# Optimization experiments

Hardware: AMD Instinct MI355X
Metric: run time of the kernel (lower is better)

Reference implementation:

```python
import jax, jax.numpy as jnp
import numpy as np
from functools import partial

B = 524288      # batch
CH = 30         # channel_num (input dim)
FEA = 42        # feature dim consumed by all classifiers
HID = 64        # assumed hidden width of the (unshown) Feature MLP
NC = 2          # num_class -> number of conditional-domain experts
ND = 6          # num_domain
ALPHA = 1.0

# Gradient Reversal Layer: identity fwd, -alpha * grad bwd
@partial(jax.custom_vjp, nondiff_argnums=(1,))
def grl(x, alpha):
    return x

def _grl_fwd(x, alpha):
    return x, None

def _grl_bwd(alpha, res, g):
    return (-alpha * g,)

grl.defvjp(_grl_fwd, _grl_bwd)


def setup_inputs() -> dict:
    key = jax.random.key(0)
    ks = jax.random.split(key, 24)
    r = lambda k, shape, s=0.1: (jax.random.normal(k, shape, dtype=jnp.float32) * s)
    inp = {
        "x": jax.random.normal(ks[0], (B, CH), dtype=jnp.float32),
        "y": jax.random.randint(ks[1], (B,), 0, NC, dtype=jnp.int32),
        # Feature MLP (assumed: CH -> HID -> FEA with ReLU)
        "W_f1": r(ks[2], (CH, HID)), "b_f1": jnp.zeros((HID,), jnp.float32),
        "W_f2": r(ks[3], (HID, FEA)), "b_f2": jnp.zeros((FEA,), jnp.float32),
        # TaskClassifier: 42 -> 20 -> NC
        "W_t1": r(ks[4], (FEA, 20)), "b_t1": jnp.zeros((20,), jnp.float32),
        "W_t2": r(ks[5], (20, NC)), "b_t2": jnp.zeros((NC,), jnp.float32),
        # prior domain classifier: 42 -> 20 -> 20 -> ND
        "W_p1": r(ks[6], (FEA, 20)), "b_p1": jnp.zeros((20,), jnp.float32),
        "W_p2": r(ks[7], (20, 20)), "b_p2": jnp.zeros((20,), jnp.float32),
        "W_p3": r(ks[8], (20, ND)), "b_p3": jnp.zeros((ND,), jnp.float32),
        # NC conditional domain experts, stacked: [NC, ...]
        "W_c1": r(ks[9], (NC, FEA, 20)), "b_c1": jnp.zeros((NC, 20), jnp.float32),
        "W_c2": r(ks[10], (NC, 20, 20)), "b_c2": jnp.zeros((NC, 20), jnp.float32),
        "W_c3": r(ks[11], (NC, 20, ND)), "b_c3": jnp.zeros((NC, ND), jnp.float32),
    }
    return inp


def reference(x, y, W_f1, b_f1, W_f2, b_f2, W_t1, b_t1, W_t2, b_t2,
              W_p1, b_p1, W_p2, b_p2, W_p3, b_p3,
              W_c1, b_c1, W_c2, b_c2, W_c3, b_c3):
    # feature extractor
    h = jax.nn.relu(x @ W_f1 + b_f1)
    fea = jax.nn.relu(h @ W_f2 + b_f2)              # [B, 42]
    # task head
    t = jax.nn.relu(fea @ W_t1 + b_t1)
    task_predict = t @ W_t2 + b_t2                   # [B, NC]
    # gradient-reversed feature for domain heads
    fr = grl(fea, ALPHA)
    # prior domain classifier
    p = jax.nn.relu(fr @ W_p1 + b_p1)
    p = jax.nn.relu(p @ W_p2 + b_p2)
    pd_predict = p @ W_p3 + b_p3                     # [B, ND]
    # conditional experts: with NC=2 compute all experts, then route by label
    c = jax.nn.relu(jnp.einsum('bf,cfh->bch', fr, W_c1) + b_c1[None])
    c = jax.nn.relu(jnp.einsum('bch,chk->bck', c, W_c2) + b_c2[None])
    cd_all = jnp.einsum('bck,ckd->bcd', c, W_c3) + b_c3[None]   # [B, NC, ND]
    cd_predicts = jnp.take_along_axis(cd_all, y[:, None, None].astype(jnp.int32), axis=1)[:, 0, :]
    return (task_predict, pd_predict, cd_predicts)
```

## Files before the change

kernel.cpp:

```cpp
#include <hip/hip_runtime.h>
#include <hip/hip_bf16.h>

typedef __bf16 bf8 __attribute__((ext_vector_type(8)));
typedef unsigned short u16x8 __attribute__((ext_vector_type(8)));
typedef float f32x4 __attribute__((ext_vector_type(4)));
typedef float f32x2 __attribute__((ext_vector_type(2)));
typedef unsigned int u32x4 __attribute__((ext_vector_type(4)));

union FragU { u16x8 u; bf8 b; u32x4 q; };
union BiasU { f32x4 f; u32x4 q; };

struct __attribute__((packed, aligned(4))) F4u { float v[4]; };
struct __attribute__((packed, aligned(4))) F2u { float v[2]; };

static __device__ __forceinline__ f32x4 MM(const FragU& a, const FragU& b, f32x4 c) {
  return __builtin_amdgcn_mfma_f32_16x16x32_bf16(a.b, b.b, c, 0, 0, 0);
}

#define NBATCH 524288
#define NCH 4
#define SPB (NCH * 16 * 4)
#define NTIL (NBATCH / SPB)
#define GRID 1024
#define ITERS (NTIL / GRID)
#define NFRAG 37

__global__ __launch_bounds__(64) void cdann_prep(
    const float* __restrict__ gWf1, const float* __restrict__ gbf1,
    const float* __restrict__ gWf2, const float* __restrict__ gbf2,
    const float* __restrict__ gWt1, const float* __restrict__ gbt1,
    const float* __restrict__ gWt2, const float* __restrict__ gbt2,
    const float* __restrict__ gWp1, const float* __restrict__ gbp1,
    const float* __restrict__ gWp2, const float* __restrict__ gbp2,
    const float* __restrict__ gWp3, const float* __restrict__ gbp3,
    const float* __restrict__ gWc1, const float* __restrict__ gbc1,
    const float* __restrict__ gWc2, const float* __restrict__ gbc2,
    const float* __restrict__ gWc3, const float* __restrict__ gbc3,
    u32x4* __restrict__ ws)
{
  const int lane = (int)threadIdx.x & 63;
  const int fid = (int)blockIdx.x;
  const int g = lane >> 4;
  const int c15 = lane & 15;

  auto colF2 = [](int nt, int m) -> int {
    if (nt < 2) return 8 * (m >> 2) + 4 * nt + (m & 3);
    const int gm = m >> 2, r = m & 3;
    if (gm == 0) return 32 + r;
    if (gm == 1) return 36 + r;
    if (gm == 2 && r < 2) return 40 + r;
    return -1;
  };

  if (fid >= 34) {
    const int nt = fid - 34;
    BiasU b;
#pragma unroll
    for (int r = 0; r < 4; ++r) {
      const int col = colF2(nt, g * 4 + r);
      b.f[r] = (col >= 0) ? gbf2[col] : 0.f;
    }
    ws[fid * 64 + lane] = b.q;
    return;
  }

  auto v_f1 = [&](int k, int m, int nt) -> float {
    const int n = 32 * (nt >> 1) + 8 * (m >> 2) + 4 * (nt & 1) + (m & 3);
    if (k < 30) return gWf1[k * 64 + n];
    if (k == 30) return gbf1[n];
    return 0.f;
  };
  auto v_f2 = [&](int k, int m, int nt) -> float {
    const int col = colF2(nt, m);
    return (col >= 0) ? gWf2[k * 42 + col] : 0.f;
  };
  auto ffea = [](int v) -> int {
    if (v < 36) return v;
    if (v == 36) return -2;
    if (v >= 40 && v <= 43) return v - 4;
    if (v == 48 || v == 49) return v - 8;
    return -1;
  };
  auto v_q = [&](int k, int m, int nt) -> float {
    const int i = ffea(k);
    if (i == -1) return 0.f;
    const int gm = m >> 2;
    const int u = 4 * nt + (m & 3);
    const int head = u / 5;
    const int f = 5 * gm + (u % 5);
    if (head == 0) return (i == -2) ? gbt1[f] : gWt1[i * 20 + f];
    if (head == 1) return (i == -2) ? gbp1[f] : gWp1[i * 20 + f];
    if (head == 2) return (i == -2) ? gbc1[f] : gWc1[i * 20 + f];
    return (i == -2) ? gbc1[20 + f] : gWc1[(42 + i) * 20 + f];
  };
  auto v_tp = [&](int k, int m, int nt) -> float {
    const int ks = k >> 5, j = k & 7, gk = (k >> 3) & 3;
    const int gm = m >> 2;
    const int u = 4 * nt + (m & 3);
    const int isP2 = (u < 5);
    const int cp = 5 * gm + u;
    const int isT2 = (!isP2 && gm == 0 && (u == 5 || u == 6));
    const int ct = u - 5;
    if (ks == 0) {
      if (j < 5) { const int i = 5 * gk + j; return isT2 ? gWt2[i * 2 + ct] : 0.f; }
      if (j == 7 && gk == 0) { if (isT2) return gbt2[ct]; if (isP2) return gbp2[cp]; }
      return 0.f;
    } else {
      if (j < 5) { const int i = 5 * gk + j; return isP2 ? gWp2[i * 20 + cp] : 0.f; }
      return 0.f;
    }
  };
  auto v_cc = [&](int k, int m, int nt) -> float {
    const int ks = k >> 5, j = k & 7, gk = (k >> 3) & 3;
    const int gm = m >> 2;
    const int u = 4 * nt + (m & 3);
    const int isE0 = (u < 5);
    const int isE1 = (u >= 5 && u < 10);
    const int c0 = 5 * gm + u;
    const int c1 = 5 * gm + (u - 5);
    if (ks == 0) {
      if (j < 5) { const int i = 5 * gk + j; return isE0 ? gWc2[i * 20 + c0] : 0.f; }
      if (j == 7 && gk == 0) { if (isE0) return gbc2[c0]; if (isE1) return gbc2[20 + c1]; }
      return 0.f;
    } else {
      if (j < 5) { const int i = 5 * gk + j; return isE1 ? gWc2[(20 + i) * 20 + c1] : 0.f; }
      return 0.f;
    }
  };
  auto v_o = [&](int k, int m, int nt) -> float {
    const int ks = k >> 5, j = k & 7, gk = (k >> 3) & 3;
    const int gm = m >> 2, r = m & 3;
    int kind = -1, c = 0;
    if (nt == 0) {
      if (gm == 0) { kind = 0; c = r; }
      else if (gm == 1) { if (r < 2) { kind = 0; c = 4 + r; } else { kind = 1; c = r - 2; } }
      else if (gm == 2) { kind = 1; c = 2 + r; }
      else { kind = 2; c = r; }
    } else {
      if (gm == 0 && r < 2) { kind = 2; c = 4 + r; }
    }
    if (kind < 0) return 0.f;
    if (ks == 0) {
      if (j < 5) { const int i = 5 * gk + j; return (kind == 0) ? gWp3[i * 6 + c] : 0.f; }
      if (j < 7) { const int i = 5 * gk + (j - 5); return (kind == 2) ? gWc3[(20 + i) * 6 + c] : 0.f; }
      if (gk == 0) {
        if (kind == 0) return gbp3[c];
        if (kind == 1) return gbc3[c];
        return gbc3[6 + c];
      }
      return 0.f;
    } else {
      if (j < 5) { const int i = 5 * gk + j; return (kind == 1) ? gWc3[i * 6 + c] : 0.f; }
      const int i = 5 * gk + 2 + (j - 5);
      return (kind == 2) ? gWc3[(20 + i) * 6 + c] : 0.f;
    }
  };

  int ks, nt, which;
  if (fid < 4)       { ks = 0;                nt = fid;            which = 0; }
  else if (fid < 10) { int t = fid - 4;  ks = t / 3; nt = t % 3;   which = 1; }
  else if (fid < 20) { int t = fid - 10; ks = t / 5; nt = t % 5;   which = 2; }
  else if (fid < 24) { int t = fid - 20; ks = t / 2; nt = t % 2;   which = 3; }
  else if (fid < 30) { int t = fid - 24; ks = t / 3; nt = t % 3;   which = 4; }
  else               { int t = fid - 30; ks = t / 2; nt = t % 2;   which = 5; }

  FragU f;
#pragma unroll
  for (int j = 0; j < 8; ++j) {
    const int k = ks * 32 + g * 8 + j;
    float v;
    switch (which) {
      case 0: v = v_f1(k, c15, nt); break;
      case 1: v = v_f2(k, c15, nt); break;
      case 2: v = v_q(k, c15, nt); break;
      case 3: v = v_tp(k, c15, nt); break;
      case 4: v = v_cc(k, c15, nt); break;
      default: v = v_o(k, c15, nt); break;
    }
    f.b[j] = (__bf16)v;
  }
  ws[fid * 64 + lane] = f.q;
}

__global__ __launch_bounds__(256, 2) void cdann_fwd(
    const float* __restrict__ gx, const int* __restrict__ gy,
    const u32x4* __restrict__ ws, float* __restrict__ gout)
{
  const int tid = (int)threadIdx.x;
  const int lane = tid & 63;
  const int w = tid >> 6;
  const int g = lane >> 4;
  const int c15 = lane & 15;

  FragU wF1[4], wF2[2][3], wQ[2][5], wTP[2][2], wCC[2][3], wO[2][2];
#pragma unroll
  for (int nt = 0; nt < 4; ++nt) wF1[nt].q = ws[nt * 64 + lane];
#pragma unroll
  for (int ks = 0; ks < 2; ++ks) {
#pragma unroll
    for (int nt = 0; nt < 3; ++nt) wF2[ks][nt].q = ws[(4 + ks * 3 + nt) * 64 + lane];
#pragma unroll
    for (int nt = 0; nt < 5; ++nt) wQ[ks][nt].q = ws[(10 + ks * 5 + nt) * 64 + lane];
#pragma unroll
    for (int nt = 0; nt < 2; ++nt) wTP[ks][nt].q = ws[(20 + ks * 2 + nt) * 64 + lane];
#pragma unroll
    for (int nt = 0; nt < 3; ++nt) wCC[ks][nt].q = ws[(24 + ks * 3 + nt) * 64 + lane];
#pragma unroll
    for (int nt = 0; nt < 2; ++nt) wO[ks][nt].q = ws[(30 + ks * 2 + nt) * 64 + lane];
  }
  f32x4 bF2[3];
#pragma unroll
  for (int nt = 0; nt < 3; ++nt) {
    BiasU b; b.q = ws[(34 + nt) * 64 + lane];
    bF2[nt] = b.f;
  }

#pragma unroll
  for (int nt = 0; nt < 4; ++nt) asm volatile("" : "+v"(wF1[nt].u));
#pragma unroll
  for (int ks = 0; ks < 2; ++ks) {
#pragma unroll
    for (int nt = 0; nt < 3; ++nt) asm volatile("" : "+v"(wF2[ks][nt].u));
#pragma unroll
    for (int nt = 0; nt < 5; ++nt) asm volatile("" : "+v"(wQ[ks][nt].u));
#pragma unroll
    for (int nt = 0; nt < 2; ++nt) asm volatile("" : "+v"(wTP[ks][nt].u));
#pragma unroll
    for (int nt = 0; nt < 3; ++nt) asm volatile("" : "+v"(wCC[ks][nt].u));
#pragma unroll
    for (int nt = 0; nt < 2; ++nt) asm volatile("" : "+v"(wO[ks][nt].u));
  }
#pragma unroll
  for (int nt = 0; nt < 3; ++nt) asm volatile("" : "+v"(bF2[nt]));

  const f32x4 zf = {0.f, 0.f, 0.f, 0.f};
  const __bf16 one = (__bf16)1.0f;
  const __bf16 zero = (__bf16)0.0f;
  float* const outT = gout;
  float* const outP = gout + (size_t)2 * NBATCH;
  float* const outC = gout + (size_t)8 * NBATCH;

  for (int ii = 0; ii < ITERS; ++ii) {
    const int it = (int)blockIdx.x + ii * GRID;
    const int base = it * SPB + w * (NCH * 16) + c15;

    float xr[NCH][8];
    int ys[NCH];
#pragma unroll
    for (int c = 0; c < NCH; ++c) {
      const int s = base + c * 16;
      const float* xp = gx + (size_t)s * 30 + g * 8;
      if (g < 3) {
        F4u a0 = *(const F4u*)xp; F4u a1 = *(const F4u*)(xp + 4);
#pragma unroll
        for (int j = 0; j < 4; ++j) { xr[c][j] = a0.v[j]; xr[c][4 + j] = a1.v[j]; }
      } else {
        F4u a0 = *(const F4u*)xp; F2u a1 = *(const F2u*)(xp + 4);
#pragma unroll
        for (int j = 0; j < 4; ++j) xr[c][j] = a0.v[j];
        xr[c][4] = a1.v[0]; xr[c][5] = a1.v[1];
        xr[c][6] = 1.0f; xr[c][7] = 0.0f;
      }
      ys[c] = gy[s];
    }

    FragU bh0[NCH], bh1[NCH];
#pragma unroll
    for (int c = 0; c < NCH; ++c) {
      FragU bx;
#pragma unroll
      for (int j = 0; j < 8; ++j) bx.b[j] = (__bf16)xr[c][j];
      f32x4 aH[4];
#pragma unroll
      for (int nt = 0; nt < 4; ++nt) aH[nt] = MM(wF1[nt], bx, zf);
#pragma unroll
      for (int j = 0; j < 8; ++j) {
        bh0[c].b[j] = (__bf16)fmaxf(aH[j >> 2][j & 3], 0.f);
        bh1[c].b[j] = (__bf16)fmaxf(aH[2 + (j >> 2)][j & 3], 0.f);
      }
    }

    FragU bf0[NCH], bf1[NCH];
#pragma unroll
    for (int c = 0; c < NCH; ++c) {
      f32x4 aF[3];
#pragma unroll
      for (int nt = 0; nt < 3; ++nt) aF[nt] = MM(wF2[1][nt], bh1[c], MM(wF2[0][nt], bh0[c], zf));
#pragma unroll
      for (int j = 0; j < 8; ++j)
        bf0[c].b[j] = (__bf16)fmaxf(aF[j >> 2][j & 3] + bF2[j >> 2][j & 3], 0.f);
#pragma unroll
      for (int j = 0; j < 4; ++j)
        bf1[c].b[j] = (__bf16)fmaxf(aF[2][j] + bF2[2][j], 0.f);
      bf1[c].b[4] = (g == 0) ? one : zero;
      bf1[c].b[5] = zero; bf1[c].b[6] = zero; bf1[c].b[7] = zero;
    }

    f32x4 aOr0[NCH], aOr1[NCH];
    f32x2 t2v[NCH];
#pragma unroll
    for (int c = 0; c < NCH; ++c) {
      f32x4 aQ[5];
#pragma unroll
      for (int nt = 0; nt < 5; ++nt) aQ[nt] = MM(wQ[1][nt], bf1[c], MM(wQ[0][nt], bf0[c], zf));
      auto rq = [&](int u) { return (__bf16)fmaxf(aQ[u >> 2][u & 3], 0.f); };
      FragU tp0, tp1, cc0, cc1;
#pragma unroll
      for (int j = 0; j < 5; ++j) {
        tp0.b[j] = rq(j);
        tp1.b[j] = rq(5 + j);
        cc0.b[j] = rq(10 + j);
        cc1.b[j] = rq(15 + j);
      }
      tp0.b[5] = zero; tp0.b[6] = zero; tp0.b[7] = (g == 0) ? one : zero;
      tp1.b[5] = zero; tp1.b[6] = zero; tp1.b[7] = zero;
      cc0.b[5] = zero; cc0.b[6] = zero; cc0.b[7] = (g == 0) ? one : zero;
      cc1.b[5] = zero; cc1.b[6] = zero; cc1.b[7] = zero;
      f32x4 aT[2], aC[3];
#pragma unroll
      for (int nt = 0; nt < 2; ++nt) aT[nt] = MM(wTP[1][nt], tp1, MM(wTP[0][nt], tp0, zf));
#pragma unroll
      for (int nt = 0; nt < 3; ++nt) aC[nt] = MM(wCC[1][nt], cc1, MM(wCC[0][nt], cc0, zf));
      FragU f50, f51;
#pragma unroll
      for (int j = 0; j < 4; ++j) {
        f50.b[j] = (__bf16)fmaxf(aT[0][j], 0.f);
        f51.b[j] = (__bf16)fmaxf(aC[0][j], 0.f);
      }
      f50.b[4] = (__bf16)fmaxf(aT[1][0], 0.f);
      f50.b[5] = (__bf16)fmaxf(aC[1][1], 0.f);
      f50.b[6] = (__bf16)fmaxf(aC[1][2], 0.f);
      f50.b[7] = (g == 0) ? one : zero;
      f51.b[4] = (__bf16)fmaxf(aC[1][0], 0.f);
      f51.b[5] = (__bf16)fmaxf(aC[1][3], 0.f);
      f51.b[6] = (__bf16)fmaxf(aC[2][0], 0.f);
      f51.b[7] = (__bf16)fmaxf(aC[2][1], 0.f);
      aOr0[c] = MM(wO[0][0], f50, zf);
      aOr0[c] = MM(wO[1][0], f51, aOr0[c]);
      aOr1[c] = MM(wO[0][1], f50, zf);
      aOr1[c] = MM(wO[1][1], f51, aOr1[c]);
      t2v[c][0] = aT[1][1]; t2v[c][1] = aT[1][2];
    }

#pragma unroll
    for (int c = 0; c < NCH; ++c) {
      const int s = base + c * 16;
      const int y = ys[c];
      const f32x4 aO0 = aOr0[c], aO1 = aOr1[c];
      if (g == 0) {
        *(f32x2*)(outT + (size_t)s * 2) = t2v[c];
        f32x2 pa = {aO0[0], aO0[1]}, pb = {aO0[2], aO0[3]};
        *(f32x2*)(outP + (size_t)s * 6) = pa;
        *(f32x2*)(outP + (size_t)s * 6 + 2) = pb;
        if (y) { f32x2 cv = {aO1[0], aO1[1]}; *(f32x2*)(outC + (size_t)s * 6 + 4) = cv; }
      } else if (g == 1) {
        f32x2 pc = {aO0[0], aO0[1]};
        *(f32x2*)(outP + (size_t)s * 6 + 4) = pc;
        if (!y) { f32x2 cv = {aO0[2], aO0[3]}; *(f32x2*)(outC + (size_t)s * 6) = cv; }
      } else if (g == 2) {
        if (!y) {
          f32x2 ca = {aO0[0], aO0[1]}, cb = {aO0[2], aO0[3]};
          *(f32x2*)(outC + (size_t)s * 6 + 2) = ca;
          *(f32x2*)(outC + (size_t)s * 6 + 4) = cb;
        }
      } else {
        if (y) {
          f32x2 ca = {aO0[0], aO0[1]}, cb = {aO0[2], aO0[3]};
          *(f32x2*)(outC + (size_t)s * 6) = ca;
          *(f32x2*)(outC + (size_t)s * 6 + 2) = cb;
        }
      }
    }
  }
}

extern "C" void kernel_launch(void* const* d_in, const int* in_sizes, int n_in,
                              void* d_out, int out_size, void* d_ws, size_t ws_size,
                              hipStream_t stream) {
  (void)in_sizes; (void)n_in; (void)ws_size; (void)out_size;
  const float* gx  = (const float*)d_in[0];
  const int*   gy  = (const int*)d_in[1];
  const float* Wf1 = (const float*)d_in[2];  const float* bf1 = (const float*)d_in[3];
  const float* Wf2 = (const float*)d_in[4];  const float* bf2 = (const float*)d_in[5];
  const float* Wt1 = (const float*)d_in[6];  const float* bt1 = (const float*)d_in[7];
  const float* Wt2 = (const float*)d_in[8];  const float* bt2 = (const float*)d_in[9];
  const float* Wp1 = (const float*)d_in[10]; const float* bp1 = (const float*)d_in[11];
  const float* Wp2 = (const float*)d_in[12]; const float* bp2 = (const float*)d_in[13];
  const float* Wp3 = (const float*)d_in[14]; const float* bp3 = (const float*)d_in[15];
  const float* Wc1 = (const float*)d_in[16]; const float* bc1 = (const float*)d_in[17];
  const float* Wc2 = (const float*)d_in[18]; const float* bc2 = (const float*)d_in[19];
  const float* Wc3 = (const float*)d_in[20]; const float* bc3 = (const float*)d_in[21];
  float* out = (float*)d_out;
  u32x4* ws = (u32x4*)d_ws;

  cdann_prep<<<dim3(NFRAG), dim3(64), 0, stream>>>(
      Wf1, bf1, Wf2, bf2, Wt1, bt1, Wt2, bt2,
      Wp1, bp1, Wp2, bp2, Wp3, bp3, Wc1, bc1, Wc2, bc2, Wc3, bc3, ws);

  cdann_fwd<<<dim3(GRID), dim3(256), 0, stream>>>(gx, gy, ws, out);
}
```

Baseline: 41.38 us.

## Stage weight fragments in LDS and software-pipeline x loads per tile

Weight fragments move from per-thread registers into a shared-memory table filled once per block. Each wave now handles a single 16-sample chunk per iteration, and the next iteration's x and y are prefetched into registers while the current one computes. Occupancy is raised to 4 blocks per SIMD. Lower register pressure should let more waves hide memory latency, in exchange for LDS reads before every MFMA and less independent MFMA work per wave.

```diff
diff --git a/kernel.cpp b/kernel.cpp
--- a/kernel.cpp
+++ b/kernel.cpp
@@ -18,8 +18,7 @@
 }
 
 #define NBATCH 524288
-#define NCH 4
-#define SPB (NCH * 16 * 4)
+#define SPB 64
 #define NTIL (NBATCH / SPB)
 #define GRID 1024
 #define ITERS (NTIL / GRID)
@@ -182,56 +181,19 @@
   ws[fid * 64 + lane] = f.q;
 }
 
-__global__ __launch_bounds__(256, 2) void cdann_fwd(
+__global__ __launch_bounds__(256, 4) void cdann_fwd(
     const float* __restrict__ gx, const int* __restrict__ gy,
     const u32x4* __restrict__ ws, float* __restrict__ gout)
 {
+  __shared__ __align__(16) u32x4 lfr[NFRAG * 64];
   const int tid = (int)threadIdx.x;
   const int lane = tid & 63;
   const int w = tid >> 6;
   const int g = lane >> 4;
   const int c15 = lane & 15;
 
-  FragU wF1[4], wF2[2][3], wQ[2][5], wTP[2][2], wCC[2][3], wO[2][2];
-#pragma unroll
-  for (int nt = 0; nt < 4; ++nt) wF1[nt].q = ws[nt * 64 + lane];
-#pragma unroll
-  for (int ks = 0; ks < 2; ++ks) {
-#pragma unroll
-    for (int nt = 0; nt < 3; ++nt) wF2[ks][nt].q = ws[(4 + ks * 3 + nt) * 64 + lane];
-#pragma unroll
-    for (int nt = 0; nt < 5; ++nt) wQ[ks][nt].q = ws[(10 + ks * 5 + nt) * 64 + lane];
-#pragma unroll
-    for (int nt = 0; nt < 2; ++nt) wTP[ks][nt].q = ws[(20 + ks * 2 + nt) * 64 + lane];
-#pragma unroll
-    for (int nt = 0; nt < 3; ++nt) wCC[ks][nt].q = ws[(24 + ks * 3 + nt) * 64 + lane];
-#pragma unroll
-    for (int nt = 0; nt < 2; ++nt) wO[ks][nt].q = ws[(30 + ks * 2 + nt) * 64 + lane];
-  }
-  f32x4 bF2[3];
-#pragma unroll
-  for (int nt = 0; nt < 3; ++nt) {
-    BiasU b; b.q = ws[(34 + nt) * 64 + lane];
-    bF2[nt] = b.f;
-  }
-
-#pragma unroll
-  for (int nt = 0; nt < 4; ++nt) asm volatile("" : "+v"(wF1[nt].u));
-#pragma unroll
-  for (int ks = 0; ks < 2; ++ks) {
-#pragma unroll
-    for (int nt = 0; nt < 3; ++nt) asm volatile("" : "+v"(wF2[ks][nt].u));
-#pragma unroll
-    for (int nt = 0; nt < 5; ++nt) asm volatile("" : "+v"(wQ[ks][nt].u));
-#pragma unroll
-    for (int nt = 0; nt < 2; ++nt) asm volatile("" : "+v"(wTP[ks][nt].u));
-#pragma unroll
-    for (int nt = 0; nt < 3; ++nt) asm volatile("" : "+v"(wCC[ks][nt].u));
-#pragma unroll
-    for (int nt = 0; nt < 2; ++nt) asm volatile("" : "+v"(wO[ks][nt].u));
-  }
-#pragma unroll
-  for (int nt = 0; nt < 3; ++nt) asm volatile("" : "+v"(bF2[nt]));
+  for (int i = tid; i < NFRAG * 64; i += 256) lfr[i] = ws[i];
+  __syncthreads();
 
   const f32x4 zf = {0.f, 0.f, 0.f, 0.f};
   const __bf16 one = (__bf16)1.0f;
@@ -240,71 +202,81 @@
   float* const outP = gout + (size_t)2 * NBATCH;
   float* const outC = gout + (size_t)8 * NBATCH;
 
+  FragU bxp;
+  int ysp;
+  auto loadx = [&](int it) {
+    const int s = it * SPB + w * 16 + c15;
+    const float* xp = gx + (size_t)s * 30 + g * 8;
+    float t[8];
+    if (g < 3) {
+      F4u a0 = *(const F4u*)xp; F4u a1 = *(const F4u*)(xp + 4);
+#pragma unroll
+      for (int j = 0; j < 4; ++j) { t[j] = a0.v[j]; t[4 + j] = a1.v[j]; }
+    } else {
+      F4u a0 = *(const F4u*)xp; F2u a1 = *(const F2u*)(xp + 4);
+#pragma unroll
+      for (int j = 0; j < 4; ++j) t[j] = a0.v[j];
+      t[4] = a1.v[0]; t[5] = a1.v[1];
+      t[6] = 1.0f; t[7] = 0.0f;
+    }
+#pragma unroll
+    for (int j = 0; j < 8; ++j) bxp.b[j] = (__bf16)t[j];
+    ysp = gy[s];
+  };
+
+  loadx((int)blockIdx.x);
+
   for (int ii = 0; ii < ITERS; ++ii) {
     const int it = (int)blockIdx.x + ii * GRID;
-    const int base = it * SPB + w * (NCH * 16) + c15;
-
-    float xr[NCH][8];
-    int ys[NCH];
-#pragma unroll
-    for (int c = 0; c < NCH; ++c) {
-      const int s = base + c * 16;
-      const float* xp = gx + (size_t)s * 30 + g * 8;
-      if (g < 3) {
-        F4u a0 = *(const F4u*)xp; F4u a1 = *(const F4u*)(xp + 4);
-#pragma unroll
-        for (int j = 0; j < 4; ++j) { xr[c][j] = a0.v[j]; xr[c][4 + j] = a1.v[j]; }
-      } else {
-        F4u a0 = *(const F4u*)xp; F2u a1 = *(const F2u*)(xp + 4);
-#pragma unroll
-        for (int j = 0; j < 4; ++j) xr[c][j] = a0.v[j];
-        xr[c][4] = a1.v[0]; xr[c][5] = a1.v[1];
-        xr[c][6] = 1.0f; xr[c][7] = 0.0f;
-      }
-      ys[c] = gy[s];
-    }
-
-    FragU bh0[NCH], bh1[NCH];
-#pragma unroll
-    for (int c = 0; c < NCH; ++c) {
-      FragU bx;
-#pragma unroll
-      for (int j = 0; j < 8; ++j) bx.b[j] = (__bf16)xr[c][j];
-      f32x4 aH[4];
-#pragma unroll
-      for (int nt = 0; nt < 4; ++nt) aH[nt] = MM(wF1[nt], bx, zf);
+    const int s = it * SPB + w * 16 + c15;
+
+    FragU bx = bxp;
+    const int y = ysp;
+
+    if (ii + 1 < ITERS) loadx(it + GRID);
+
+    int ofs = lane;
+    asm volatile("" : "+v"(ofs));
+    auto LF = [&](int fid) { FragU t; t.q = lfr[fid * 64 + ofs]; return t; };
+
+    f32x4 aH[4];
+#pragma unroll
+    for (int nt = 0; nt < 4; ++nt) aH[nt] = MM(LF(nt), bx, zf);
+    FragU bh0, bh1;
+#pragma unroll
+    for (int j = 0; j < 8; ++j) {
+      bh0.b[j] = (__bf16)fmaxf(aH[j >> 2][j & 3], 0.f);
+      bh1.b[j] = (__bf16)fmaxf(aH[2 + (j >> 2)][j & 3], 0.f);
+    }
+
+    f32x4 aF[3];
+#pragma unroll
+    for (int nt = 0; nt < 3; ++nt)
+      aF[nt] = MM(LF(7 + nt), bh1, MM(LF(4 + nt), bh0, zf));
+    FragU bf0, bf1;
+    {
+      BiasU b0, b1, b2;
+      b0.q = lfr[34 * 64 + ofs]; b1.q = lfr[35 * 64 + ofs]; b2.q = lfr[36 * 64 + ofs];
 #pragma unroll
       for (int j = 0; j < 8; ++j) {
-        bh0[c].b[j] = (__bf16)fmaxf(aH[j >> 2][j & 3], 0.f);
-        bh1[c].b[j] = (__bf16)fmaxf(aH[2 + (j >> 2)][j & 3], 0.f);
-      }
-    }
-
-    FragU bf0[NCH], bf1[NCH];
-#pragma unroll
-    for (int c = 0; c < NCH; ++c) {
-      f32x4 aF[3];
-#pragma unroll
-      for (int nt = 0; nt < 3; ++nt) aF[nt] = MM(wF2[1][nt], bh1[c], MM(wF2[0][nt], bh0[c], zf));
-#pragma unroll
-      for (int j = 0; j < 8; ++j)
-        bf0[c].b[j] = (__bf16)fmaxf(aF[j >> 2][j & 3] + bF2[j >> 2][j & 3], 0.f);
+        const float bb = (j >> 2) ? b1.f[j & 3] : b0.f[j & 3];
+        bf0.b[j] = (__bf16)fmaxf(aF[j >> 2][j & 3] + bb, 0.f);
+      }
 #pragma unroll
       for (int j = 0; j < 4; ++j)
-        bf1[c].b[j] = (__bf16)fmaxf(aF[2][j] + bF2[2][j], 0.f);
-      bf1[c].b[4] = (g == 0) ? one : zero;
-      bf1[c].b[5] = zero; bf1[c].b[6] = zero; bf1[c].b[7] = zero;
-    }
-
-    f32x4 aOr0[NCH], aOr1[NCH];
-    f32x2 t2v[NCH];
-#pragma unroll
-    for (int c = 0; c < NCH; ++c) {
-      f32x4 aQ[5];
-#pragma unroll
-      for (int nt = 0; nt < 5; ++nt) aQ[nt] = MM(wQ[1][nt], bf1[c], MM(wQ[0][nt], bf0[c], zf));
+        bf1.b[j] = (__bf16)fmaxf(aF[2][j] + b2.f[j], 0.f);
+      bf1.b[4] = (g == 0) ? one : zero;
+      bf1.b[5] = zero; bf1.b[6] = zero; bf1.b[7] = zero;
+    }
+
+    f32x4 aQ[5];
+#pragma unroll
+    for (int nt = 0; nt < 5; ++nt)
+      aQ[nt] = MM(LF(15 + nt), bf1, MM(LF(10 + nt), bf0, zf));
+    FragU tp0, tp1, cc0, cc1;
+    {
+      const __bf16 c1v = (g == 0) ? one : zero;
       auto rq = [&](int u) { return (__bf16)fmaxf(aQ[u >> 2][u & 3], 0.f); };
-      FragU tp0, tp1, cc0, cc1;
 #pragma unroll
       for (int j = 0; j < 5; ++j) {
         tp0.b[j] = rq(j);
@@ -312,63 +284,62 @@
         cc0.b[j] = rq(10 + j);
         cc1.b[j] = rq(15 + j);
       }
-      tp0.b[5] = zero; tp0.b[6] = zero; tp0.b[7] = (g == 0) ? one : zero;
+      tp0.b[5] = zero; tp0.b[6] = zero; tp0.b[7] = c1v;
       tp1.b[5] = zero; tp1.b[6] = zero; tp1.b[7] = zero;
-      cc0.b[5] = zero; cc0.b[6] = zero; cc0.b[7] = (g == 0) ? one : zero;
+      cc0.b[5] = zero; cc0.b[6] = zero; cc0.b[7] = c1v;
       cc1.b[5] = zero; cc1.b[6] = zero; cc1.b[7] = zero;
-      f32x4 aT[2], aC[3];
-#pragma unroll
-      for (int nt = 0; nt < 2; ++nt) aT[nt] = MM(wTP[1][nt], tp1, MM(wTP[0][nt], tp0, zf));
-#pragma unroll
-      for (int nt = 0; nt < 3; ++nt) aC[nt] = MM(wCC[1][nt], cc1, MM(wCC[0][nt], cc0, zf));
-      FragU f50, f51;
-#pragma unroll
-      for (int j = 0; j < 4; ++j) {
-        f50.b[j] = (__bf16)fmaxf(aT[0][j], 0.f);
-        f51.b[j] = (__bf16)fmaxf(aC[0][j], 0.f);
-      }
-      f50.b[4] = (__bf16)fmaxf(aT[1][0], 0.f);
-      f50.b[5] = (__bf16)fmaxf(aC[1][1], 0.f);
-      f50.b[6] = (__bf16)fmaxf(aC[1][2], 0.f);
-      f50.b[7] = (g == 0) ? one : zero;
-      f51.b[4] = (__bf16)fmaxf(aC[1][0], 0.f);
-      f51.b[5] = (__bf16)fmaxf(aC[1][3], 0.f);
-      f51.b[6] = (__bf16)fmaxf(aC[2][0], 0.f);
-      f51.b[7] = (__bf16)fmaxf(aC[2][1], 0.f);
-      aOr0[c] = MM(wO[0][0], f50, zf);
-      aOr0[c] = MM(wO[1][0], f51, aOr0[c]);
-      aOr1[c] = MM(wO[0][1], f50, zf);
-      aOr1[c] = MM(wO[1][1], f51, aOr1[c]);
-      t2v[c][0] = aT[1][1]; t2v[c][1] = aT[1][2];
-    }
-
-#pragma unroll
-    for (int c = 0; c < NCH; ++c) {
-      const int s = base + c * 16;
-      const int y = ys[c];
-      const f32x4 aO0 = aOr0[c], aO1 = aOr1[c];
-      if (g == 0) {
-        *(f32x2*)(outT + (size_t)s * 2) = t2v[c];
-        f32x2 pa = {aO0[0], aO0[1]}, pb = {aO0[2], aO0[3]};
-        *(f32x2*)(outP + (size_t)s * 6) = pa;
-        *(f32x2*)(outP + (size_t)s * 6 + 2) = pb;
-        if (y) { f32x2 cv = {aO1[0], aO1[1]}; *(f32x2*)(outC + (size_t)s * 6 + 4) = cv; }
-      } else if (g == 1) {
-        f32x2 pc = {aO0[0], aO0[1]};
-        *(f32x2*)(outP + (size_t)s * 6 + 4) = pc;
-        if (!y) { f32x2 cv = {aO0[2], aO0[3]}; *(f32x2*)(outC + (size_t)s * 6) = cv; }
-      } else if (g == 2) {
-        if (!y) {
-          f32x2 ca = {aO0[0], aO0[1]}, cb = {aO0[2], aO0[3]};
-          *(f32x2*)(outC + (size_t)s * 6 + 2) = ca;
-          *(f32x2*)(outC + (size_t)s * 6 + 4) = cb;
-        }
-      } else {
-        if (y) {
-          f32x2 ca = {aO0[0], aO0[1]}, cb = {aO0[2], aO0[3]};
-          *(f32x2*)(outC + (size_t)s * 6) = ca;
-          *(f32x2*)(outC + (size_t)s * 6 + 2) = cb;
-        }
+    }
+
+    f32x4 aT[2];
+#pragma unroll
+    for (int nt = 0; nt < 2; ++nt)
+      aT[nt] = MM(LF(22 + nt), tp1, MM(LF(20 + nt), tp0, zf));
+    f32x4 aC[3];
+#pragma unroll
+    for (int nt = 0; nt < 3; ++nt)
+      aC[nt] = MM(LF(27 + nt), cc1, MM(LF(24 + nt), cc0, zf));
+
+    FragU f50, f51;
+    f32x2 t2v;
+#pragma unroll
+    for (int j = 0; j < 4; ++j) {
+      f50.b[j] = (__bf16)fmaxf(aT[0][j], 0.f);
+      f51.b[j] = (__bf16)fmaxf(aC[0][j], 0.f);
+    }
+    f50.b[4] = (__bf16)fmaxf(aT[1][0], 0.f);
+    f50.b[5] = (__bf16)fmaxf(aC[1][1], 0.f);
+    f50.b[6] = (__bf16)fmaxf(aC[1][2], 0.f);
+    f50.b[7] = (g == 0) ? one : zero;
+    f51.b[4] = (__bf16)fmaxf(aC[1][0], 0.f);
+    f51.b[5] = (__bf16)fmaxf(aC[1][3], 0.f);
+    f51.b[6] = (__bf16)fmaxf(aC[2][0], 0.f);
+    f51.b[7] = (__bf16)fmaxf(aC[2][1], 0.f);
+    t2v[0] = aT[1][1]; t2v[1] = aT[1][2];
+
+    f32x4 aO0 = MM(LF(32), f51, MM(LF(30), f50, zf));
+    f32x4 aO1 = MM(LF(33), f51, MM(LF(31), f50, zf));
+
+    if (g == 0) {
+      *(f32x2*)(outT + (size_t)s * 2) = t2v;
+      f32x2 pa = {aO0[0], aO0[1]}, pb = {aO0[2], aO0[3]};
+      *(f32x2*)(outP + (size_t)s * 6) = pa;
+      *(f32x2*)(outP + (size_t)s * 6 + 2) = pb;
+      if (y) { f32x2 cv = {aO1[0], aO1[1]}; *(f32x2*)(outC + (size_t)s * 6 + 4) = cv; }
+    } else if (g == 1) {
+      f32x2 pc = {aO0[0], aO0[1]};
+      *(f32x2*)(outP + (size_t)s * 6 + 4) = pc;
+      if (!y) { f32x2 cv = {aO0[2], aO0[3]}; *(f32x2*)(outC + (size_t)s * 6) = cv; }
+    } else if (g == 2) {
+      if (!y) {
+        f32x2 ca = {aO0[0], aO0[1]}, cb = {aO0[2], aO0[3]};
+        *(f32x2*)(outC + (size_t)s * 6 + 2) = ca;
+        *(f32x2*)(outC + (size_t)s * 6 + 4) = cb;
+      }
+    } else {
+      if (y) {
+        f32x2 ca = {aO0[0], aO0[1]}, cb = {aO0[2], aO0[3]};
+        *(f32x2*)(outC + (size_t)s * 6) = ca;
+        *(f32x2*)(outC + (size_t)s * 6 + 2) = cb;
       }
     }
   }
```

Result: faster. 38.73 us (-6.4%).
